# Performance work log

Measured on AMD Instinct MI355X. Metric: run time of the kernel, lower is better.

The kernel has to match this reference:

```python
import jax, jax.numpy as jnp
import numpy as np

N_NODES = 100000
N_EDGES = 1600000
NODE_DIM = 32
EDGE_DIM = 8
NUM_LAYERS = 3
NEG_SLOPE = 0.01  # F.leaky_relu default
EPS = 0.0         # GINEConv default eps, train_eps=False


def setup_inputs() -> dict:
    key = jax.random.key(0)
    ks = jax.random.split(key, 7)
    x = jax.random.normal(ks[0], (N_NODES, NODE_DIM), dtype=jnp.float32)
    edge_attr = jax.random.normal(ks[1], (N_EDGES, EDGE_DIM), dtype=jnp.float32)
    W = jax.random.normal(ks[2], (NUM_LAYERS, NODE_DIM, NODE_DIM), dtype=jnp.float32) / np.sqrt(NODE_DIM)
    b = jax.random.normal(ks[3], (NUM_LAYERS, NODE_DIM), dtype=jnp.float32) * 0.01
    We = jax.random.normal(ks[4], (NUM_LAYERS, EDGE_DIM, NODE_DIM), dtype=jnp.float32) / np.sqrt(EDGE_DIM)
    be = jax.random.normal(ks[5], (NUM_LAYERS, NODE_DIM), dtype=jnp.float32) * 0.01
    edge_index = jax.random.randint(ks[6], (2, N_EDGES), 0, N_NODES, dtype=jnp.int64 if jax.config.jax_enable_x64 else jnp.int32)
    return {"x": x, "edge_attr": edge_attr, "W": W, "b": b, "We": We, "be": be,
            "edge_index": edge_index}


def reference(x, edge_attr, W, b, We, be, edge_index):
    # 3 stacked GINEConv layers + leaky_relu, PyG semantics:
    # out = Linear((1+eps)*x_i + sum_{j->i} ReLU(x_j + Lin_e(edge_attr_ji)))
    src = edge_index[0]  # source nodes j
    dst = edge_index[1]  # target nodes i
    n = x.shape[0]
    for l in range(NUM_LAYERS):
        e = edge_attr @ We[l] + be[l]                       # [E, D] edge embedding
        msg = jax.nn.relu(x[src] + e)                        # gather + message
        agg = jax.ops.segment_sum(msg, dst, num_segments=n)  # scatter-add
        h = (1.0 + EPS) * x + agg
        x = jax.nn.leaky_relu(h @ W[l] + b[l], negative_slope=NEG_SLOPE)
    return x
```

## Files before the change

### kernel.cpp

```cpp
#include <hip/hip_runtime.h>

#define N_NODES 100000
#define N_EDGES 1600000
#define D 32
#define ED 8
#define NEG_SLOPE 0.01f
#define CB 782
#define BKN 128
#define A_EPB 8192
#define A_NB ((N_EDGES + A_EPB - 1) / A_EPB)
#define NBLK 98

typedef unsigned int uint;
typedef unsigned short ushort;
typedef __fp16 half2v __attribute__((ext_vector_type(2)));

__device__ __forceinline__ uint bf16_rne(float f) {
    uint u = __float_as_uint(f);
    return (u + 0x7fffu + ((u >> 16) & 1u)) >> 16;
}
__device__ __forceinline__ uint pack2(float lo, float hi) {
    return bf16_rne(lo) | (bf16_rne(hi) << 16);
}
__device__ __forceinline__ float bf_lo(uint u) { return __uint_as_float(u << 16); }
__device__ __forceinline__ float bf_hi(uint u) { return __uint_as_float(u & 0xffff0000u); }
__device__ __forceinline__ float bf_us(ushort u) { return __uint_as_float(((uint)u) << 16); }

__device__ __forceinline__ uint ph2(float lo, float hi) {
    __fp16 l = (__fp16)lo, h = (__fp16)hi;
    return (uint)__builtin_bit_cast(ushort, l) | ((uint)__builtin_bit_cast(ushort, h) << 16);
}

#if defined(__has_builtin) && __has_builtin(__builtin_amdgcn_fdot2)
__device__ __forceinline__ float fdot2f(uint u, half2v w, float c) {
    return __builtin_amdgcn_fdot2(__builtin_bit_cast(half2v, u), w, c, false);
}
#else
__device__ __forceinline__ float fdot2f(uint u, half2v w, float c) {
    half2v a = __builtin_bit_cast(half2v, u);
    return c + (float)a.x * (float)w.x + (float)a.y * (float)w.y;
}
#endif

__global__ __launch_bounds__(256) void pack_x_kernel(
    const float* __restrict__ x, ushort* __restrict__ xb)
{
    int i = blockIdx.x * 256 + threadIdx.x;
    if (i >= N_NODES * D / 4) return;
    float4 f = ((const float4*)x)[i];
    ((uint2*)xb)[i] = make_uint2(pack2(f.x, f.y), pack2(f.z, f.w));
}

__global__ __launch_bounds__(256) void countA_kernel(
    const int* __restrict__ dst, int* __restrict__ cntM)
{
    __shared__ int h[CB];
    const int t = threadIdx.x;
    for (int i = t; i < CB; i += 256) h[i] = 0;
    __syncthreads();
    const int e0 = blockIdx.x * A_EPB;
    for (int j = 0; j < A_EPB; j += 256) {
        int e = e0 + j + t;
        if (e < N_EDGES) atomicAdd(&h[dst[e] >> 7], 1);
    }
    __syncthreads();
    for (int i = t; i < CB; i += 256) cntM[blockIdx.x * CB + i] = h[i];
}

__global__ __launch_bounds__(256) void scanS1_kernel(
    const int* __restrict__ cntM, int* __restrict__ exclM, int* __restrict__ btot)
{
    __shared__ int s[256];
    const int t = threadIdx.x;
    const int b = blockIdx.x;
    int v = (t < A_NB) ? cntM[t * CB + b] : 0;
    s[t] = v;
    __syncthreads();
    for (int off = 1; off < 256; off <<= 1) {
        int u = (t >= off) ? s[t - off] : 0;
        __syncthreads();
        s[t] += u;
        __syncthreads();
    }
    if (t < A_NB) exclM[t * CB + b] = s[t] - v;
    if (t == 255) btot[b] = s[255];
}

__global__ __launch_bounds__(1024) void scanS2_kernel(
    const int* __restrict__ btot, int* __restrict__ bbase, int* __restrict__ row_ptr)
{
    __shared__ int s[1024];
    const int t = threadIdx.x;
    int v = (t < CB) ? btot[t] : 0;
    s[t] = v;
    __syncthreads();
    for (int off = 1; off < 1024; off <<= 1) {
        int u = (t >= off) ? s[t - off] : 0;
        __syncthreads();
        s[t] += u;
        __syncthreads();
    }
    if (t < CB) bbase[t] = s[t] - v;
    if (t == 0) row_ptr[N_NODES] = N_EDGES;
}

__global__ __launch_bounds__(256) void scatterA_kernel(
    const int*   __restrict__ src,
    const int*   __restrict__ dst,
    const float* __restrict__ edge_attr,
    const int*   __restrict__ exclM,
    const int*   __restrict__ bbase,
    uint*        __restrict__ rec_tmp)
{
    __shared__ int cur[CB];
    const int t = threadIdx.x;
    for (int i = t; i < CB; i += 256)
        cur[i] = bbase[i] + exclM[blockIdx.x * CB + i];
    __syncthreads();
    const int e0 = blockIdx.x * A_EPB;
    const float4* ea4 = (const float4*)edge_attr;
    for (int j = 0; j < A_EPB; j += 256) {
        int e = e0 + j + t;
        if (e >= N_EDGES) continue;
        int dn = dst[e];
        int pos = atomicAdd(&cur[dn >> 7], 1);
        float4 a = ea4[(long)e * 2];
        float4 c = ea4[(long)e * 2 + 1];
        uint* r = rec_tmp + (size_t)pos * 8;
        *(uint4*)r = make_uint4(ph2(a.x, a.y), ph2(a.z, a.w),
                                ph2(c.x, c.y), ph2(c.z, c.w));
        *(uint2*)(r + 4) = make_uint2((uint)src[e], (uint)dn);
    }
}

__global__ __launch_bounds__(256) void fineB_kernel(
    const uint* __restrict__ rec_tmp,
    const int*  __restrict__ bbase,
    int*        __restrict__ row_ptr,
    uint4*      __restrict__ ea16,
    int*        __restrict__ srcf)
{
    __shared__ int h[BKN];
    __shared__ int ex[BKN];
    const int t = threadIdx.x;
    const int b = blockIdx.x;
    const int e0 = bbase[b];
    const int e1 = (b == CB - 1) ? N_EDGES : bbase[b + 1];

    if (t < BKN) h[t] = 0;
    __syncthreads();
    for (int r = e0 + t; r < e1; r += 256)
        atomicAdd(&h[rec_tmp[(size_t)r * 8 + 5] & (BKN - 1)], 1);
    __syncthreads();
    if (t < BKN) ex[t] = h[t];
    __syncthreads();
    for (int off = 1; off < BKN; off <<= 1) {
        int u = (t < BKN && t >= off) ? ex[t - off] : 0;
        __syncthreads();
        if (t < BKN) ex[t] += u;
        __syncthreads();
    }
    if (t < BKN) {
        int excl = ex[t] - h[t];
        int n = b * BKN + t;
        if (n < N_NODES) row_ptr[n] = e0 + excl;
        h[t] = e0 + excl;
    }
    __syncthreads();
    for (int r = e0 + t; r < e1; r += 256) {
        const uint* rt = rec_tmp + (size_t)r * 8;
        uint4 ea = *(const uint4*)rt;
        uint2 sd = *(const uint2*)(rt + 4);
        int pos = atomicAdd(&h[sd.y & (BKN - 1)], 1);
        ea16[pos] = ea;
        srcf[pos] = (int)sd.x;
    }
}

__global__ __launch_bounds__(256) void gine_fused4_kernel(
    const ushort* __restrict__ xb_in, ushort* __restrict__ xb_out,
    float* __restrict__ f32_out, const int* __restrict__ row_ptr,
    const uint4* __restrict__ ea16, const int* __restrict__ srcf,
    const float* __restrict__ W, const float* __restrict__ b,
    const float* __restrict__ We, const float* __restrict__ be)
{
    __shared__ float W_s[D * D];
    const int t = threadIdx.x;
    for (int i = t; i < D * D; i += 256) W_s[i] = W[i];

    const int n = blockIdx.x * 8 + (t >> 5);
    const int d = t & 31;

    half2v wep[4];
#pragma unroll
    for (int k = 0; k < 4; ++k) {
        wep[k].x = (__fp16)We[(2 * k) * D + d];
        wep[k].y = (__fp16)We[(2 * k + 1) * D + d];
    }
    const float bed = be[d];
    const float bd  = b[d];
    __syncthreads();
    if (n >= N_NODES) return;

    const int row = row_ptr[n], rend = row_ptr[n + 1];
    float selfx = bf_us(xb_in[n * D + d]);

    float acc = 0.0f;
    int pos = row;
    for (; pos + 4 <= rend; pos += 4) {
        uint4 ev[4];
        int sj[4];
#pragma unroll
        for (int j = 0; j < 4; ++j) {
            ev[j] = ea16[pos + j];
            sj[j] = srcf[pos + j];
        }
        float xv[4];
#pragma unroll
        for (int j = 0; j < 4; ++j)
            xv[j] = bf_us(xb_in[sj[j] * D + d]);
#pragma unroll
        for (int j = 0; j < 4; ++j) {
            float e = fdot2f(ev[j].w, wep[3],
                      fdot2f(ev[j].z, wep[2],
                      fdot2f(ev[j].y, wep[1],
                      fdot2f(ev[j].x, wep[0], bed))));
            acc += fmaxf(xv[j] + e, 0.0f);
        }
    }
    if (pos < rend) {
        const int rem = rend - pos;
        uint4 ev[4];
        int sj[4];
#pragma unroll
        for (int j = 0; j < 4; ++j) {
            int idx = pos + ((j < rem) ? j : 0);
            ev[j] = ea16[idx];
            sj[j] = srcf[idx];
        }
        float xv[4];
#pragma unroll
        for (int j = 0; j < 4; ++j)
            xv[j] = bf_us(xb_in[sj[j] * D + d]);
#pragma unroll
        for (int j = 0; j < 4; ++j) {
            float e = fdot2f(ev[j].w, wep[3],
                      fdot2f(ev[j].z, wep[2],
                      fdot2f(ev[j].y, wep[1],
                      fdot2f(ev[j].x, wep[0], bed))));
            float msg = fmaxf(xv[j] + e, 0.0f);
            acc += (j < rem) ? msg : 0.0f;
        }
    }

    float h = selfx + acc;
    float o = bd;
#pragma unroll
    for (int k = 0; k < D; ++k)
        o += __shfl(h, k, 32) * W_s[k * D + d];
    o = o > 0.0f ? o : NEG_SLOPE * o;
    xb_out[n * D + d] = (ushort)bf16_rne(o);
    if (f32_out) f32_out[n * D + d] = o;
}

__global__ __launch_bounds__(256) void hist_kernel(
    const int* __restrict__ dst, int* __restrict__ deg)
{
    int i = blockIdx.x * 256 + threadIdx.x;
    if (i >= N_EDGES / 4) return;
    int4 dd = ((const int4*)dst)[i];
    atomicAdd(&deg[dd.x], 1);
    atomicAdd(&deg[dd.y], 1);
    atomicAdd(&deg[dd.z], 1);
    atomicAdd(&deg[dd.w], 1);
}

__global__ __launch_bounds__(1024) void scan_phase1(
    const int* __restrict__ deg, int* __restrict__ bsums)
{
    __shared__ int s[1024];
    int t = threadIdx.x;
    int i = blockIdx.x * 1024 + t;
    s[t] = (i < N_NODES) ? deg[i] : 0;
    __syncthreads();
    for (int off = 512; off > 0; off >>= 1) {
        if (t < off) s[t] += s[t + off];
        __syncthreads();
    }
    if (t == 0) bsums[blockIdx.x] = s[0];
}

__global__ __launch_bounds__(128) void scan_phase2(int* __restrict__ bsums)
{
    __shared__ int s[128];
    int t = threadIdx.x;
    int v = (t < NBLK) ? bsums[t] : 0;
    s[t] = v;
    __syncthreads();
    for (int off = 1; off < 128; off <<= 1) {
        int u = (t >= off) ? s[t - off] : 0;
        __syncthreads();
        s[t] += u;
        __syncthreads();
    }
    if (t < NBLK) bsums[t] = s[t] - v;
}

__global__ __launch_bounds__(1024) void scan_phase3(
    const int* __restrict__ deg, const int* __restrict__ bsums,
    int* __restrict__ row_ptr, int* __restrict__ offs)
{
    __shared__ int s[1024];
    int t = threadIdx.x;
    int i = blockIdx.x * 1024 + t;
    int v = (i < N_NODES) ? deg[i] : 0;
    s[t] = v;
    __syncthreads();
    for (int off = 1; off < 1024; off <<= 1) {
        int u = (t >= off) ? s[t - off] : 0;
        __syncthreads();
        s[t] += u;
        __syncthreads();
    }
    int excl = bsums[blockIdx.x] + s[t] - v;
    if (i < N_NODES) { row_ptr[i] = excl; offs[i] = excl; }
    else if (i == N_NODES) row_ptr[i] = excl;
}

__global__ __launch_bounds__(256) void scatter_rec_kernel(
    const int* __restrict__ src, const int* __restrict__ dst,
    const float* __restrict__ edge_attr, int* __restrict__ offs,
    uint* __restrict__ rec)
{
    int e = blockIdx.x * 256 + threadIdx.x;
    if (e >= N_EDGES) return;
    int pos = atomicAdd(&offs[dst[e]], 1);
    const float4* ea4 = (const float4*)edge_attr;
    float4 a = ea4[(long)e * 2];
    float4 c = ea4[(long)e * 2 + 1];
    uint* r = rec + (long)pos * 8;
    *(uint4*)r = make_uint4((uint)src[e], pack2(a.x, a.y), pack2(a.z, a.w), pack2(c.x, c.y));
    r[4] = pack2(c.z, c.w);
}

__global__ __launch_bounds__(256) void gine_fused2_kernel(
    const ushort* __restrict__ xb_in, ushort* __restrict__ xb_out,
    float* __restrict__ f32_out, const int* __restrict__ row_ptr,
    const uint* __restrict__ rec,
    const float* __restrict__ W, const float* __restrict__ b,
    const float* __restrict__ We, const float* __restrict__ be)
{
    __shared__ float W_s[D * D];
    __shared__ float We_s[ED * D];
    __shared__ float b_s[D];
    __shared__ float be_s[D];
    const int t = threadIdx.x;
    for (int i = t; i < D * D; i += 256) W_s[i] = W[i];
    if (t < ED * D) We_s[t] = We[t];
    if (t < D) { b_s[t] = b[t]; be_s[t] = be[t]; }
    __syncthreads();
    const int n = blockIdx.x * 8 + (t >> 5);
    const int d = t & 31;
    if (n >= N_NODES) return;
    float wer[ED];
#pragma unroll
    for (int k = 0; k < ED; ++k) wer[k] = We_s[k * D + d];
    const float bed = be_s[d];
    const int row = row_ptr[n], rend = row_ptr[n + 1];
    float selfx = bf_us(xb_in[n * D + d]);
    float acc = 0.0f;
    for (int pos = row; pos < rend; pos += 8) {
        const int rem = rend - pos;
        const uint2* rp = (const uint2*)(rec + (long)pos * 8);
        uint2 v = rp[d];
        int srcs[8];
#pragma unroll
        for (int j = 0; j < 8; ++j) srcs[j] = __shfl((int)v.x, 4 * j, 32);
        const int s0 = srcs[0];
        float xv[8];
#pragma unroll
        for (int j = 0; j < 8; ++j) {
            int sj = (j < rem) ? srcs[j] : s0;
            xv[j] = bf_us(xb_in[sj * D + d]);
        }
#pragma unroll
        for (int j = 0; j < 8; ++j) {
            uint u01 = (uint)__shfl((int)v.y, 4 * j, 32);
            uint u23 = (uint)__shfl((int)v.x, 4 * j + 1, 32);
            uint u45 = (uint)__shfl((int)v.y, 4 * j + 1, 32);
            uint u67 = (uint)__shfl((int)v.x, 4 * j + 2, 32);
            float e = bed;
            e += bf_lo(u01) * wer[0]; e += bf_hi(u01) * wer[1];
            e += bf_lo(u23) * wer[2]; e += bf_hi(u23) * wer[3];
            e += bf_lo(u45) * wer[4]; e += bf_hi(u45) * wer[5];
            e += bf_lo(u67) * wer[6]; e += bf_hi(u67) * wer[7];
            float msg = fmaxf(xv[j] + e, 0.0f);
            acc += (j < rem) ? msg : 0.0f;
        }
    }
    float h = selfx + acc;
    float o = b_s[d];
#pragma unroll
    for (int k = 0; k < D; ++k)
        o += __shfl(h, k, 32) * W_s[k * D + d];
    o = o > 0.0f ? o : NEG_SLOPE * o;
    xb_out[n * D + d] = (ushort)bf16_rne(o);
    if (f32_out) f32_out[n * D + d] = o;
}

__global__ __launch_bounds__(256) void gine_edge_kernel(
    const float* __restrict__ x, const float* __restrict__ edge_attr,
    const float* __restrict__ We, const float* __restrict__ be,
    const int* __restrict__ src, const int* __restrict__ dst,
    float* __restrict__ agg)
{
    __shared__ float We_s[ED * D];
    __shared__ float be_s[D];
    int t = threadIdx.x;
    if (t < ED * D) We_s[t] = We[t];
    if (t < D) be_s[t] = be[t];
    __syncthreads();
    long gtid = (long)blockIdx.x * blockDim.x + t;
    int e = (int)(gtid >> 5), d = (int)(gtid & 31);
    if (e >= N_EDGES) return;
    int s = src[e], dn = dst[e];
    float acc = be_s[d];
#pragma unroll
    for (int k = 0; k < ED; ++k)
        acc += edge_attr[(long)e * ED + k] * We_s[k * D + d];
    float m = fmaxf(x[(long)s * D + d] + acc, 0.0f);
    atomicAdd(&agg[(long)dn * D + d], m);
}

__global__ __launch_bounds__(256) void gine_node_kernel(
    float* __restrict__ x, const float* __restrict__ agg,
    const float* __restrict__ W, const float* __restrict__ b)
{
    __shared__ float W_s[D * D];
    __shared__ float b_s[D];
    int t = threadIdx.x;
    for (int i = t; i < D * D; i += 256) W_s[i] = W[i];
    if (t < D) b_s[t] = b[t];
    __syncthreads();
    long gtid = (long)blockIdx.x * blockDim.x + t;
    int n = (int)(gtid >> 5), d = (int)(gtid & 31);
    if (n >= N_NODES) return;
    float h = x[(long)n * D + d] + agg[(long)n * D + d];
    float acc = b_s[d];
#pragma unroll
    for (int k = 0; k < D; ++k)
        acc += __shfl(h, k, D) * W_s[k * D + d];
    x[(long)n * D + d] = acc > 0.0f ? acc : NEG_SLOPE * acc;
}

extern "C" void kernel_launch(void* const* d_in, const int* in_sizes, int n_in,
                              void* d_out, int out_size, void* d_ws, size_t ws_size,
                              hipStream_t stream) {
    const float* x_in      = (const float*)d_in[0];
    const float* edge_attr = (const float*)d_in[1];
    const float* W         = (const float*)d_in[2];
    const float* b         = (const float*)d_in[3];
    const float* We        = (const float*)d_in[4];
    const float* be        = (const float*)d_in[5];
    const int*   ei        = (const int*)d_in[6];
    const int* src = ei;
    const int* dst = ei + N_EDGES;

    const size_t xbytes  = (size_t)N_NODES * D * sizeof(float);
    const size_t xbbytes = (size_t)N_NODES * D * sizeof(ushort);

    auto align = [](size_t v) { return (v + 255) & ~(size_t)255; };
    size_t off_xba  = 0;
    size_t off_rp   = align(off_xba + xbbytes);
    size_t off_cnt  = align(off_rp + (N_NODES + 1) * sizeof(int));
    size_t off_excl = align(off_cnt + (size_t)A_NB * CB * sizeof(int));
    size_t off_bt   = align(off_excl + (size_t)A_NB * CB * sizeof(int));
    size_t off_bb   = align(off_bt + CB * sizeof(int));
    size_t off_ea   = align(off_bb + CB * sizeof(int));
    size_t off_src  = align(off_ea + ((size_t)N_EDGES + 8) * 16);
    size_t off_rtmp = align(off_src + ((size_t)N_EDGES + 8) * 4);
    size_t need_big = off_rtmp + (size_t)N_EDGES * 32 + 256;
    size_t off_mrec = off_ea;
    size_t off_mxbb = align(off_mrec + ((size_t)N_EDGES + 8) * 32);
    size_t need_mid = off_mxbb + xbbytes + 256;

    char* ws = (char*)d_ws;
    ushort* xbA    = (ushort*)(ws + off_xba);
    int*   row_ptr = (int*)   (ws + off_rp);
    int*   cntM    = (int*)   (ws + off_cnt);
    int*   exclM   = (int*)   (ws + off_excl);
    int*   btot    = (int*)   (ws + off_bt);
    int*   bbase   = (int*)   (ws + off_bb);
    uint4* ea16    = (uint4*) (ws + off_ea);
    int*   srcf    = (int*)   (ws + off_src);
    uint*  rec_tmp = (uint*)  (ws + off_rtmp);
    ushort* xbB    = (ushort*)(ws + off_rtmp);
    float* xout    = (float*)d_out;

    if (ws_size >= need_big) {
        pack_x_kernel<<<(N_NODES * D / 4 + 255) / 256, 256, 0, stream>>>(x_in, xbA);
        countA_kernel<<<A_NB, 256, 0, stream>>>(dst, cntM);
        scanS1_kernel<<<CB, 256, 0, stream>>>(cntM, exclM, btot);
        scanS2_kernel<<<1, 1024, 0, stream>>>(btot, bbase, row_ptr);
        scatterA_kernel<<<A_NB, 256, 0, stream>>>(src, dst, edge_attr, exclM, bbase, rec_tmp);
        fineB_kernel<<<CB, 256, 0, stream>>>(rec_tmp, bbase, row_ptr, ea16, srcf);

        dim3 blk(256), grid((N_NODES + 7) / 8);
        gine_fused4_kernel<<<grid, blk, 0, stream>>>(xbA, xbB, nullptr, row_ptr, ea16, srcf,
            W, b, We, be);
        gine_fused4_kernel<<<grid, blk, 0, stream>>>(xbB, xbA, nullptr, row_ptr, ea16, srcf,
            W + D * D, b + D, We + ED * D, be + D);
        gine_fused4_kernel<<<grid, blk, 0, stream>>>(xbA, xbB, xout, row_ptr, ea16, srcf,
            W + 2 * D * D, b + 2 * D, We + 2 * ED * D, be + 2 * D);
    } else if (ws_size >= need_mid) {
        int* deg  = cntM;
        int* offs = exclM;
        int* bsums = btot;
        uint* rec = (uint*)(ws + off_mrec);
        ushort* xbBm = (ushort*)(ws + off_mxbb);
        pack_x_kernel<<<(N_NODES * D / 4 + 255) / 256, 256, 0, stream>>>(x_in, xbA);
        hipMemsetAsync(deg, 0, N_NODES * sizeof(int), stream);
        hist_kernel<<<(N_EDGES / 4 + 255) / 256, 256, 0, stream>>>(dst, deg);
        scan_phase1<<<NBLK, 1024, 0, stream>>>(deg, bsums);
        scan_phase2<<<1, 128, 0, stream>>>(bsums);
        scan_phase3<<<NBLK, 1024, 0, stream>>>(deg, bsums, row_ptr, offs);
        scatter_rec_kernel<<<(N_EDGES + 255) / 256, 256, 0, stream>>>(
            src, dst, edge_attr, offs, rec);
        dim3 blk(256), grid((N_NODES + 7) / 8);
        gine_fused2_kernel<<<grid, blk, 0, stream>>>(xbA, xbBm, nullptr, row_ptr, rec,
            W, b, We, be);
        gine_fused2_kernel<<<grid, blk, 0, stream>>>(xbBm, xbA, nullptr, row_ptr, rec,
            W + D * D, b + D, We + ED * D, be + D);
        gine_fused2_kernel<<<grid, blk, 0, stream>>>(xbA, xbBm, xout, row_ptr, rec,
            W + 2 * D * D, b + 2 * D, We + 2 * ED * D, be + 2 * D);
    } else {
        float* x = (float*)d_out;
        float* agg = (float*)d_ws;
        hipMemcpyAsync(x, x_in, xbytes, hipMemcpyDeviceToDevice, stream);
        dim3 eblk(256), egrid(((long)N_EDGES * D + 255) / 256);
        dim3 nblk(256), ngrid(((long)N_NODES * D + 255) / 256);
        for (int l = 0; l < 3; ++l) {
            hipMemsetAsync(agg, 0, xbytes, stream);
            gine_edge_kernel<<<egrid, eblk, 0, stream>>>(
                x, edge_attr, We + (size_t)l * ED * D, be + (size_t)l * D, src, dst, agg);
            gine_node_kernel<<<ngrid, nblk, 0, stream>>>(
                x, agg, W + (size_t)l * D * D, b + (size_t)l * D);
        }
    }
}
```

Measured before the change: 403.8 us.

## Split scatter temp records into SoA arrays and shrink edges-per-block for scatter

Splits the 32-byte intermediate edge record into a 16-byte edge-attribute array and a 4-byte packed src/local-dst word, cutting temporary write and read traffic between the coarse scatter and the fine bucketing passes. The first-pass histogram also reads only the 4-byte word instead of strided records. Edges per block for the count and scatter kernels drop from 8192 to 2048, giving four times as many blocks for more parallelism. That makes the per-block count matrix and the column scan larger, so the scan kernel moves to 1024 threads. The packed word assumes source indices fit in 20 bits.

```diff
diff --git a/kernel.cpp b/kernel.cpp
--- a/kernel.cpp
+++ b/kernel.cpp
@@ -7,7 +7,7 @@
 #define NEG_SLOPE 0.01f
 #define CB 782
 #define BKN 128
-#define A_EPB 8192
+#define A_EPB 2048
 #define A_NB ((N_EDGES + A_EPB - 1) / A_EPB)
 #define NBLK 98
 
@@ -67,23 +67,23 @@
     for (int i = t; i < CB; i += 256) cntM[blockIdx.x * CB + i] = h[i];
 }
 
-__global__ __launch_bounds__(256) void scanS1_kernel(
+__global__ __launch_bounds__(1024) void scanS1_kernel(
     const int* __restrict__ cntM, int* __restrict__ exclM, int* __restrict__ btot)
 {
-    __shared__ int s[256];
+    __shared__ int s[1024];
     const int t = threadIdx.x;
     const int b = blockIdx.x;
     int v = (t < A_NB) ? cntM[t * CB + b] : 0;
     s[t] = v;
     __syncthreads();
-    for (int off = 1; off < 256; off <<= 1) {
+    for (int off = 1; off < 1024; off <<= 1) {
         int u = (t >= off) ? s[t - off] : 0;
         __syncthreads();
         s[t] += u;
         __syncthreads();
     }
     if (t < A_NB) exclM[t * CB + b] = s[t] - v;
-    if (t == 255) btot[b] = s[255];
+    if (t == 1023) btot[b] = s[1023];
 }
 
 __global__ __launch_bounds__(1024) void scanS2_kernel(
@@ -110,7 +110,8 @@
     const float* __restrict__ edge_attr,
     const int*   __restrict__ exclM,
     const int*   __restrict__ bbase,
-    uint*        __restrict__ rec_tmp)
+    uint4*       __restrict__ ea_tmp,
+    uint*        __restrict__ sd_tmp)
 {
     __shared__ int cur[CB];
     const int t = threadIdx.x;
@@ -126,19 +127,19 @@
         int pos = atomicAdd(&cur[dn >> 7], 1);
         float4 a = ea4[(long)e * 2];
         float4 c = ea4[(long)e * 2 + 1];
-        uint* r = rec_tmp + (size_t)pos * 8;
-        *(uint4*)r = make_uint4(ph2(a.x, a.y), ph2(a.z, a.w),
-                                ph2(c.x, c.y), ph2(c.z, c.w));
-        *(uint2*)(r + 4) = make_uint2((uint)src[e], (uint)dn);
+        ea_tmp[pos] = make_uint4(ph2(a.x, a.y), ph2(a.z, a.w),
+                                 ph2(c.x, c.y), ph2(c.z, c.w));
+        sd_tmp[pos] = (uint)src[e] | ((uint)(dn & (BKN - 1)) << 20);
     }
 }
 
 __global__ __launch_bounds__(256) void fineB_kernel(
-    const uint* __restrict__ rec_tmp,
-    const int*  __restrict__ bbase,
-    int*        __restrict__ row_ptr,
-    uint4*      __restrict__ ea16,
-    int*        __restrict__ srcf)
+    const uint4* __restrict__ ea_tmp,
+    const uint*  __restrict__ sd_tmp,
+    const int*   __restrict__ bbase,
+    int*         __restrict__ row_ptr,
+    uint4*       __restrict__ ea16,
+    int*         __restrict__ srcf)
 {
     __shared__ int h[BKN];
     __shared__ int ex[BKN];
@@ -150,7 +151,7 @@
     if (t < BKN) h[t] = 0;
     __syncthreads();
     for (int r = e0 + t; r < e1; r += 256)
-        atomicAdd(&h[rec_tmp[(size_t)r * 8 + 5] & (BKN - 1)], 1);
+        atomicAdd(&h[sd_tmp[r] >> 20], 1);
     __syncthreads();
     if (t < BKN) ex[t] = h[t];
     __syncthreads();
@@ -168,12 +169,11 @@
     }
     __syncthreads();
     for (int r = e0 + t; r < e1; r += 256) {
-        const uint* rt = rec_tmp + (size_t)r * 8;
-        uint4 ea = *(const uint4*)rt;
-        uint2 sd = *(const uint2*)(rt + 4);
-        int pos = atomicAdd(&h[sd.y & (BKN - 1)], 1);
+        uint sd = sd_tmp[r];
+        uint4 ea = ea_tmp[r];
+        int pos = atomicAdd(&h[sd >> 20], 1);
         ea16[pos] = ea;
-        srcf[pos] = (int)sd.x;
+        srcf[pos] = (int)(sd & 0xFFFFFu);
     }
 }
 
@@ -478,8 +478,9 @@
     size_t off_bb   = align(off_bt + CB * sizeof(int));
     size_t off_ea   = align(off_bb + CB * sizeof(int));
     size_t off_src  = align(off_ea + ((size_t)N_EDGES + 8) * 16);
-    size_t off_rtmp = align(off_src + ((size_t)N_EDGES + 8) * 4);
-    size_t need_big = off_rtmp + (size_t)N_EDGES * 32 + 256;
+    size_t off_eat  = align(off_src + ((size_t)N_EDGES + 8) * 4);
+    size_t off_sdt  = align(off_eat + ((size_t)N_EDGES + 8) * 16);
+    size_t need_big = off_sdt + ((size_t)N_EDGES + 8) * 4 + 256;
     size_t off_mrec = off_ea;
     size_t off_mxbb = align(off_mrec + ((size_t)N_EDGES + 8) * 32);
     size_t need_mid = off_mxbb + xbbytes + 256;
@@ -493,17 +494,19 @@
     int*   bbase   = (int*)   (ws + off_bb);
     uint4* ea16    = (uint4*) (ws + off_ea);
     int*   srcf    = (int*)   (ws + off_src);
-    uint*  rec_tmp = (uint*)  (ws + off_rtmp);
-    ushort* xbB    = (ushort*)(ws + off_rtmp);
+    uint4* ea_tmp  = (uint4*) (ws + off_eat);
+    uint*  sd_tmp  = (uint*)  (ws + off_sdt);
+    ushort* xbB    = (ushort*)(ws + off_eat);
     float* xout    = (float*)d_out;
 
     if (ws_size >= need_big) {
         pack_x_kernel<<<(N_NODES * D / 4 + 255) / 256, 256, 0, stream>>>(x_in, xbA);
         countA_kernel<<<A_NB, 256, 0, stream>>>(dst, cntM);
-        scanS1_kernel<<<CB, 256, 0, stream>>>(cntM, exclM, btot);
+        scanS1_kernel<<<CB, 1024, 0, stream>>>(cntM, exclM, btot);
         scanS2_kernel<<<1, 1024, 0, stream>>>(btot, bbase, row_ptr);
-        scatterA_kernel<<<A_NB, 256, 0, stream>>>(src, dst, edge_attr, exclM, bbase, rec_tmp);
-        fineB_kernel<<<CB, 256, 0, stream>>>(rec_tmp, bbase, row_ptr, ea16, srcf);
+        scatterA_kernel<<<A_NB, 256, 0, stream>>>(src, dst, edge_attr, exclM, bbase,
+                                                  ea_tmp, sd_tmp);
+        fineB_kernel<<<CB, 256, 0, stream>>>(ea_tmp, sd_tmp, bbase, row_ptr, ea16, srcf);
 
         dim3 blk(256), grid((N_NODES + 7) / 8);
         gine_fused4_kernel<<<grid, blk, 0, stream>>>(xbA, xbB, nullptr, row_ptr, ea16, srcf,
```

After: 388.7 us. -3.7%, faster.

## Replace two-pass bucketed CSR build with histogram-scan and direct atomic scatter

Applied to the files above, without the earlier changes.

Swaps the two-level radix-style CSR construction (coarse bucket count, scan, scatter to a temp record buffer, then a fine per-bucket sort) for a global degree histogram, a three-phase prefix scan, and a single scatter that uses global atomics on per-node offsets to write the bf16 edge attributes and sources straight into SoA arrays. This removes the 32-byte-per-edge temporary pass and the second reordering kernel. In exchange, edge order within each node becomes nondeterministic, and the scatter relies on contended global atomics with random writes. The workspace layout is reorganised so xbB gets its own region.

```diff
diff --git a/kernel.cpp b/kernel.cpp
--- a/kernel.cpp
+++ b/kernel.cpp
@@ -5,10 +5,6 @@
 #define D 32
 #define ED 8
 #define NEG_SLOPE 0.01f
-#define CB 782
-#define BKN 128
-#define A_EPB 8192
-#define A_NB ((N_EDGES + A_EPB - 1) / A_EPB)
 #define NBLK 98
 
 typedef unsigned int uint;
@@ -51,47 +47,57 @@
     ((uint2*)xb)[i] = make_uint2(pack2(f.x, f.y), pack2(f.z, f.w));
 }
 
-__global__ __launch_bounds__(256) void countA_kernel(
-    const int* __restrict__ dst, int* __restrict__ cntM)
-{
-    __shared__ int h[CB];
-    const int t = threadIdx.x;
-    for (int i = t; i < CB; i += 256) h[i] = 0;
-    __syncthreads();
-    const int e0 = blockIdx.x * A_EPB;
-    for (int j = 0; j < A_EPB; j += 256) {
-        int e = e0 + j + t;
-        if (e < N_EDGES) atomicAdd(&h[dst[e] >> 7], 1);
-    }
-    __syncthreads();
-    for (int i = t; i < CB; i += 256) cntM[blockIdx.x * CB + i] = h[i];
-}
-
-__global__ __launch_bounds__(256) void scanS1_kernel(
-    const int* __restrict__ cntM, int* __restrict__ exclM, int* __restrict__ btot)
-{
-    __shared__ int s[256];
-    const int t = threadIdx.x;
-    const int b = blockIdx.x;
-    int v = (t < A_NB) ? cntM[t * CB + b] : 0;
+__global__ __launch_bounds__(256) void hist_kernel(
+    const int* __restrict__ dst, int* __restrict__ deg)
+{
+    int i = blockIdx.x * 256 + threadIdx.x;
+    if (i >= N_EDGES / 4) return;
+    int4 dd = ((const int4*)dst)[i];
+    atomicAdd(&deg[dd.x], 1);
+    atomicAdd(&deg[dd.y], 1);
+    atomicAdd(&deg[dd.z], 1);
+    atomicAdd(&deg[dd.w], 1);
+}
+
+__global__ __launch_bounds__(1024) void scan_phase1(
+    const int* __restrict__ deg, int* __restrict__ bsums)
+{
+    __shared__ int s[1024];
+    int t = threadIdx.x;
+    int i = blockIdx.x * 1024 + t;
+    s[t] = (i < N_NODES) ? deg[i] : 0;
+    __syncthreads();
+    for (int off = 512; off > 0; off >>= 1) {
+        if (t < off) s[t] += s[t + off];
+        __syncthreads();
+    }
+    if (t == 0) bsums[blockIdx.x] = s[0];
+}
+
+__global__ __launch_bounds__(128) void scan_phase2(int* __restrict__ bsums)
+{
+    __shared__ int s[128];
+    int t = threadIdx.x;
+    int v = (t < NBLK) ? bsums[t] : 0;
     s[t] = v;
     __syncthreads();
-    for (int off = 1; off < 256; off <<= 1) {
+    for (int off = 1; off < 128; off <<= 1) {
         int u = (t >= off) ? s[t - off] : 0;
         __syncthreads();
         s[t] += u;
         __syncthreads();
     }
-    if (t < A_NB) exclM[t * CB + b] = s[t] - v;
-    if (t == 255) btot[b] = s[255];
-}
-
-__global__ __launch_bounds__(1024) void scanS2_kernel(
-    const int* __restrict__ btot, int* __restrict__ bbase, int* __restrict__ row_ptr)
+    if (t < NBLK) bsums[t] = s[t] - v;
+}
+
+__global__ __launch_bounds__(1024) void scan_phase3(
+    const int* __restrict__ deg, const int* __restrict__ bsums,
+    int* __restrict__ row_ptr, int* __restrict__ offs)
 {
     __shared__ int s[1024];
-    const int t = threadIdx.x;
-    int v = (t < CB) ? btot[t] : 0;
+    int t = threadIdx.x;
+    int i = blockIdx.x * 1024 + t;
+    int v = (i < N_NODES) ? deg[i] : 0;
     s[t] = v;
     __syncthreads();
     for (int off = 1; off < 1024; off <<= 1) {
@@ -100,81 +106,25 @@
         s[t] += u;
         __syncthreads();
     }
-    if (t < CB) bbase[t] = s[t] - v;
-    if (t == 0) row_ptr[N_NODES] = N_EDGES;
-}
-
-__global__ __launch_bounds__(256) void scatterA_kernel(
-    const int*   __restrict__ src,
-    const int*   __restrict__ dst,
-    const float* __restrict__ edge_attr,
-    const int*   __restrict__ exclM,
-    const int*   __restrict__ bbase,
-    uint*        __restrict__ rec_tmp)
-{
-    __shared__ int cur[CB];
-    const int t = threadIdx.x;
-    for (int i = t; i < CB; i += 256)
-        cur[i] = bbase[i] + exclM[blockIdx.x * CB + i];
-    __syncthreads();
-    const int e0 = blockIdx.x * A_EPB;
+    int excl = bsums[blockIdx.x] + s[t] - v;
+    if (i < N_NODES) { row_ptr[i] = excl; offs[i] = excl; }
+    else if (i == N_NODES) row_ptr[i] = excl;
+}
+
+__global__ __launch_bounds__(256) void scatter_soa_kernel(
+    const int* __restrict__ src, const int* __restrict__ dst,
+    const float* __restrict__ edge_attr, int* __restrict__ offs,
+    uint4* __restrict__ ea16, int* __restrict__ srcf)
+{
+    int e = blockIdx.x * 256 + threadIdx.x;
+    if (e >= N_EDGES) return;
     const float4* ea4 = (const float4*)edge_attr;
-    for (int j = 0; j < A_EPB; j += 256) {
-        int e = e0 + j + t;
-        if (e >= N_EDGES) continue;
-        int dn = dst[e];
-        int pos = atomicAdd(&cur[dn >> 7], 1);
-        float4 a = ea4[(long)e * 2];
-        float4 c = ea4[(long)e * 2 + 1];
-        uint* r = rec_tmp + (size_t)pos * 8;
-        *(uint4*)r = make_uint4(ph2(a.x, a.y), ph2(a.z, a.w),
-                                ph2(c.x, c.y), ph2(c.z, c.w));
-        *(uint2*)(r + 4) = make_uint2((uint)src[e], (uint)dn);
-    }
-}
-
-__global__ __launch_bounds__(256) void fineB_kernel(
-    const uint* __restrict__ rec_tmp,
-    const int*  __restrict__ bbase,
-    int*        __restrict__ row_ptr,
-    uint4*      __restrict__ ea16,
-    int*        __restrict__ srcf)
-{
-    __shared__ int h[BKN];
-    __shared__ int ex[BKN];
-    const int t = threadIdx.x;
-    const int b = blockIdx.x;
-    const int e0 = bbase[b];
-    const int e1 = (b == CB - 1) ? N_EDGES : bbase[b + 1];
-
-    if (t < BKN) h[t] = 0;
-    __syncthreads();
-    for (int r = e0 + t; r < e1; r += 256)
-        atomicAdd(&h[rec_tmp[(size_t)r * 8 + 5] & (BKN - 1)], 1);
-    __syncthreads();
-    if (t < BKN) ex[t] = h[t];
-    __syncthreads();
-    for (int off = 1; off < BKN; off <<= 1) {
-        int u = (t < BKN && t >= off) ? ex[t - off] : 0;
-        __syncthreads();
-        if (t < BKN) ex[t] += u;
-        __syncthreads();
-    }
-    if (t < BKN) {
-        int excl = ex[t] - h[t];
-        int n = b * BKN + t;
-        if (n < N_NODES) row_ptr[n] = e0 + excl;
-        h[t] = e0 + excl;
-    }
-    __syncthreads();
-    for (int r = e0 + t; r < e1; r += 256) {
-        const uint* rt = rec_tmp + (size_t)r * 8;
-        uint4 ea = *(const uint4*)rt;
-        uint2 sd = *(const uint2*)(rt + 4);
-        int pos = atomicAdd(&h[sd.y & (BKN - 1)], 1);
-        ea16[pos] = ea;
-        srcf[pos] = (int)sd.x;
-    }
+    float4 a = ea4[(long)e * 2];
+    float4 c = ea4[(long)e * 2 + 1];
+    int pos = atomicAdd(&offs[dst[e]], 1);
+    ea16[pos] = make_uint4(ph2(a.x, a.y), ph2(a.z, a.w),
+                           ph2(c.x, c.y), ph2(c.z, c.w));
+    srcf[pos] = src[e];
 }
 
 __global__ __launch_bounds__(256) void gine_fused4_kernel(
@@ -261,70 +211,6 @@
     o = o > 0.0f ? o : NEG_SLOPE * o;
     xb_out[n * D + d] = (ushort)bf16_rne(o);
     if (f32_out) f32_out[n * D + d] = o;
-}
-
-__global__ __launch_bounds__(256) void hist_kernel(
-    const int* __restrict__ dst, int* __restrict__ deg)
-{
-    int i = blockIdx.x * 256 + threadIdx.x;
-    if (i >= N_EDGES / 4) return;
-    int4 dd = ((const int4*)dst)[i];
-    atomicAdd(&deg[dd.x], 1);
-    atomicAdd(&deg[dd.y], 1);
-    atomicAdd(&deg[dd.z], 1);
-    atomicAdd(&deg[dd.w], 1);
-}
-
-__global__ __launch_bounds__(1024) void scan_phase1(
-    const int* __restrict__ deg, int* __restrict__ bsums)
-{
-    __shared__ int s[1024];
-    int t = threadIdx.x;
-    int i = blockIdx.x * 1024 + t;
-    s[t] = (i < N_NODES) ? deg[i] : 0;
-    __syncthreads();
-    for (int off = 512; off > 0; off >>= 1) {
-        if (t < off) s[t] += s[t + off];
-        __syncthreads();
-    }
-    if (t == 0) bsums[blockIdx.x] = s[0];
-}
-
-__global__ __launch_bounds__(128) void scan_phase2(int* __restrict__ bsums)
-{
-    __shared__ int s[128];
-    int t = threadIdx.x;
-    int v = (t < NBLK) ? bsums[t] : 0;
-    s[t] = v;
-    __syncthreads();
-    for (int off = 1; off < 128; off <<= 1) {
-        int u = (t >= off) ? s[t - off] : 0;
-        __syncthreads();
-        s[t] += u;
-        __syncthreads();
-    }
-    if (t < NBLK) bsums[t] = s[t] - v;
-}
-
-__global__ __launch_bounds__(1024) void scan_phase3(
-    const int* __restrict__ deg, const int* __restrict__ bsums,
-    int* __restrict__ row_ptr, int* __restrict__ offs)
-{
-    __shared__ int s[1024];
-    int t = threadIdx.x;
-    int i = blockIdx.x * 1024 + t;
-    int v = (i < N_NODES) ? deg[i] : 0;
-    s[t] = v;
-    __syncthreads();
-    for (int off = 1; off < 1024; off <<= 1) {
-        int u = (t >= off) ? s[t - off] : 0;
-        __syncthreads();
-        s[t] += u;
-        __syncthreads();
-    }
-    int excl = bsums[blockIdx.x] + s[t] - v;
-    if (i < N_NODES) { row_ptr[i] = excl; offs[i] = excl; }
-    else if (i == N_NODES) row_ptr[i] = excl;
 }
 
 __global__ __launch_bounds__(256) void scatter_rec_kernel(
@@ -471,39 +357,37 @@
 
     auto align = [](size_t v) { return (v + 255) & ~(size_t)255; };
     size_t off_xba  = 0;
-    size_t off_rp   = align(off_xba + xbbytes);
-    size_t off_cnt  = align(off_rp + (N_NODES + 1) * sizeof(int));
-    size_t off_excl = align(off_cnt + (size_t)A_NB * CB * sizeof(int));
-    size_t off_bt   = align(off_excl + (size_t)A_NB * CB * sizeof(int));
-    size_t off_bb   = align(off_bt + CB * sizeof(int));
-    size_t off_ea   = align(off_bb + CB * sizeof(int));
+    size_t off_xbb  = align(off_xba + xbbytes);
+    size_t off_rp   = align(off_xbb + xbbytes);
+    size_t off_deg  = align(off_rp + (N_NODES + 1) * sizeof(int));
+    size_t off_offs = align(off_deg + N_NODES * sizeof(int));
+    size_t off_bs   = align(off_offs + N_NODES * sizeof(int));
+    size_t off_ea   = align(off_bs + 1024 * sizeof(int));
     size_t off_src  = align(off_ea + ((size_t)N_EDGES + 8) * 16);
-    size_t off_rtmp = align(off_src + ((size_t)N_EDGES + 8) * 4);
-    size_t need_big = off_rtmp + (size_t)N_EDGES * 32 + 256;
+    size_t need_big = off_src + ((size_t)N_EDGES + 8) * 4 + 256;
     size_t off_mrec = off_ea;
-    size_t off_mxbb = align(off_mrec + ((size_t)N_EDGES + 8) * 32);
-    size_t need_mid = off_mxbb + xbbytes + 256;
+    size_t need_mid = align(off_mrec + ((size_t)N_EDGES + 8) * 32) + 256;
 
     char* ws = (char*)d_ws;
     ushort* xbA    = (ushort*)(ws + off_xba);
+    ushort* xbB    = (ushort*)(ws + off_xbb);
     int*   row_ptr = (int*)   (ws + off_rp);
-    int*   cntM    = (int*)   (ws + off_cnt);
-    int*   exclM   = (int*)   (ws + off_excl);
-    int*   btot    = (int*)   (ws + off_bt);
-    int*   bbase   = (int*)   (ws + off_bb);
+    int*   deg     = (int*)   (ws + off_deg);
+    int*   offs    = (int*)   (ws + off_offs);
+    int*   bsums   = (int*)   (ws + off_bs);
     uint4* ea16    = (uint4*) (ws + off_ea);
     int*   srcf    = (int*)   (ws + off_src);
-    uint*  rec_tmp = (uint*)  (ws + off_rtmp);
-    ushort* xbB    = (ushort*)(ws + off_rtmp);
     float* xout    = (float*)d_out;
 
     if (ws_size >= need_big) {
         pack_x_kernel<<<(N_NODES * D / 4 + 255) / 256, 256, 0, stream>>>(x_in, xbA);
-        countA_kernel<<<A_NB, 256, 0, stream>>>(dst, cntM);
-        scanS1_kernel<<<CB, 256, 0, stream>>>(cntM, exclM, btot);
-        scanS2_kernel<<<1, 1024, 0, stream>>>(btot, bbase, row_ptr);
-        scatterA_kernel<<<A_NB, 256, 0, stream>>>(src, dst, edge_attr, exclM, bbase, rec_tmp);
-        fineB_kernel<<<CB, 256, 0, stream>>>(rec_tmp, bbase, row_ptr, ea16, srcf);
+        hipMemsetAsync(deg, 0, N_NODES * sizeof(int), stream);
+        hist_kernel<<<(N_EDGES / 4 + 255) / 256, 256, 0, stream>>>(dst, deg);
+        scan_phase1<<<NBLK, 1024, 0, stream>>>(deg, bsums);
+        scan_phase2<<<1, 128, 0, stream>>>(bsums);
+        scan_phase3<<<NBLK, 1024, 0, stream>>>(deg, bsums, row_ptr, offs);
+        scatter_soa_kernel<<<(N_EDGES + 255) / 256, 256, 0, stream>>>(
+            src, dst, edge_attr, offs, ea16, srcf);
 
         dim3 blk(256), grid((N_NODES + 7) / 8);
         gine_fused4_kernel<<<grid, blk, 0, stream>>>(xbA, xbB, nullptr, row_ptr, ea16, srcf,
@@ -513,11 +397,7 @@
         gine_fused4_kernel<<<grid, blk, 0, stream>>>(xbA, xbB, xout, row_ptr, ea16, srcf,
             W + 2 * D * D, b + 2 * D, We + 2 * ED * D, be + 2 * D);
     } else if (ws_size >= need_mid) {
-        int* deg  = cntM;
-        int* offs = exclM;
-        int* bsums = btot;
         uint* rec = (uint*)(ws + off_mrec);
-        ushort* xbBm = (ushort*)(ws + off_mxbb);
         pack_x_kernel<<<(N_NODES * D / 4 + 255) / 256, 256, 0, stream>>>(x_in, xbA);
         hipMemsetAsync(deg, 0, N_NODES * sizeof(int), stream);
         hist_kernel<<<(N_EDGES / 4 + 255) / 256, 256, 0, stream>>>(dst, deg);
@@ -527,11 +407,11 @@
         scatter_rec_kernel<<<(N_EDGES + 255) / 256, 256, 0, stream>>>(
             src, dst, edge_attr, offs, rec);
         dim3 blk(256), grid((N_NODES + 7) / 8);
-        gine_fused2_kernel<<<grid, blk, 0, stream>>>(xbA, xbBm, nullptr, row_ptr, rec,
+        gine_fused2_kernel<<<grid, blk, 0, stream>>>(xbA, xbB, nullptr, row_ptr, rec,
             W, b, We, be);
-        gine_fused2_kernel<<<grid, blk, 0, stream>>>(xbBm, xbA, nullptr, row_ptr, rec,
+        gine_fused2_kernel<<<grid, blk, 0, stream>>>(xbB, xbA, nullptr, row_ptr, rec,
             W + D * D, b + D, We + ED * D, be + D);
-        gine_fused2_kernel<<<grid, blk, 0, stream>>>(xbA, xbBm, xout, row_ptr, rec,
+        gine_fused2_kernel<<<grid, blk, 0, stream>>>(xbA, xbB, xout, row_ptr, rec,
             W + 2 * D * D, b + 2 * D, We + 2 * ED * D, be + 2 * D);
     } else {
         float* x = (float*)d_out;
```

After: 457.3 us. 1.13x slower.
